# Kernel tuning notes

Measured on AMD Instinct MI355X. Metric: run time of the kernel, lower is better.

The kernel has to match this reference:

```python
import jax, jax.numpy as jnp
import numpy as np

N, T, I_TEXT, H, P = 64, 1024, 512, 512, 256


def setup_inputs() -> dict:
    key = jax.random.key(0)
    ks = jax.random.split(key, 7)
    s = 0.05  # keep recurrent dynamics stable
    return {
        "text_encoding": jax.random.normal(ks[0], (N, T, I_TEXT), jnp.float32),
        "text_lengths": jnp.full((N,), T, dtype=jnp.int32),
        "W_ih": jax.random.normal(ks[1], (3 * H, I_TEXT + P), jnp.float32) * s,
        "W_hh": jax.random.normal(ks[2], (3 * H, H), jnp.float32) * s,
        "b_ih": jax.random.normal(ks[3], (3 * H,), jnp.float32) * s,
        "b_hh": jax.random.normal(ks[4], (3 * H,), jnp.float32) * s,
        "W_p": jax.random.normal(ks[5], (P, H), jnp.float32) * s,
        "b_p": jax.random.normal(ks[6], (P,), jnp.float32) * s,
    }


def reference(text_encoding, text_lengths, W_ih, W_hh, b_ih, b_hh, W_p, b_p):
    n, t, _ = text_encoding.shape
    h_dim = W_hh.shape[1]
    p_dim = W_p.shape[0]
    xs = jnp.transpose(text_encoding, (1, 0, 2))  # [T, N, I_text]

    def step(carry, x):
        h, prev = carry  # h: [N,H] GRU hidden, prev: [N,P] last projected prosody vec
        inp = jnp.concatenate([x, prev], axis=-1)          # [N, I_text+P]
        gi = inp @ W_ih.T + b_ih                           # [N, 3H]
        gh = h @ W_hh.T + b_hh                             # [N, 3H]
        i_r, i_z, i_n = jnp.split(gi, 3, axis=-1)
        h_r, h_z, h_n = jnp.split(gh, 3, axis=-1)
        r = jax.nn.sigmoid(i_r + h_r)
        z = jax.nn.sigmoid(i_z + h_z)
        g = jnp.tanh(i_n + r * h_n)
        h_new = (1.0 - z) * g + z * h
        pred = h_new @ W_p.T + b_p                         # [N, P]
        return (h_new, pred), pred

    h0 = jnp.zeros((n, h_dim), text_encoding.dtype)
    p0 = jnp.zeros((n, p_dim), text_encoding.dtype)
    _, preds = jax.lax.scan(step, (h0, p0), xs)            # [T, N, P]
    return jnp.transpose(preds, (1, 0, 2))                 # [N, T, P]
```

## Files before the change

### kernel.cpp

```cpp
#include <hip/hip_runtime.h>
#include <hip/hip_bf16.h>


typedef short short8 __attribute__((ext_vector_type(8)));
typedef float f32x4 __attribute__((ext_vector_type(4)));

__device__ __forceinline__ unsigned short f2bf(float f) {
  __hip_bfloat16 h = __float2bfloat16(f);
  return *reinterpret_cast<unsigned short*>(&h);
}

__global__ void k_zero(unsigned int* __restrict__ p, int n) {
  int i = blockIdx.x * 256 + threadIdx.x;
  if (i < n) p[i] = 0u;
}

__global__ void k_fold(const float* __restrict__ W_ih, const float* __restrict__ W_hh,
                       const float* __restrict__ W_p, const float* __restrict__ b_p,
                       float* __restrict__ W_big, float* __restrict__ v_bp) {
  int idx = blockIdx.x * 256 + threadIdx.x;
  int i = idx >> 9;
  int j = idx & 511;
  const float* wip = W_ih + (long)i * 768 + 512;
  float q = 0.f;
  for (int k = 0; k < 256; ++k) q = fmaf(wip[k], W_p[k * 512 + j], q);
  if (i < 1024) {
    W_big[(long)i * 512 + j] = W_hh[(long)i * 512 + j] + q;
  } else {
    W_big[(long)i * 512 + j] = q;
    W_big[(long)(i + 512) * 512 + j] = W_hh[(long)i * 512 + j];
  }
  if (j == 0) {
    float s = 0.f;
    for (int k = 0; k < 256; ++k) s = fmaf(b_p[k], wip[k], s);
    v_bp[i] = s;
  }
}

__global__ void k_pack(const float* __restrict__ W_big, const float* __restrict__ W_ih,
                       const float* __restrict__ W_p,
                       unsigned short* __restrict__ Wr, unsigned short* __restrict__ Wx) {
  long e = (long)blockIdx.x * 256 + threadIdx.x;
  if (e < 1572864) {
    int k = (int)(e & 511);
    int cc = (int)((e >> 9) & 15);
    int rest = (int)(e >> 13);
    int T = rest % 3, b = rest / 3;
    int j = b * 8 + (cc & 7);
    bool hi = cc >= 8;
    float v;
    if (T == 0)      v = W_big[(long)(hi ? 512 + j : j) * 512 + k];
    else if (T == 1) v = W_big[(long)(hi ? 1536 + j : 1024 + j) * 512 + k];
    else             v = (cc < 4) ? W_p[(long)(b * 4 + cc) * 512 + k] : 0.f;
    Wr[e] = f2bf(v);
  } else {
    long e2 = e - 1572864;
    int g = (int)(e2 >> 9), k = (int)(e2 & 511);
    Wx[e2] = f2bf(W_ih[(long)g * 768 + k]);
  }
}

__global__ __launch_bounds__(256, 1) void k_persist(
    const float* __restrict__ x,
    const unsigned short* __restrict__ Wr, const unsigned short* __restrict__ Wx,
    const float* __restrict__ b_ih, const float* __restrict__ b_hh,
    const float* __restrict__ v_bp, const float* __restrict__ b_p,
    unsigned short* __restrict__ Hbf,
    float* __restrict__ gix,
    float* __restrict__ out,
    unsigned int* __restrict__ flags,
    unsigned int* __restrict__ gen, unsigned int* __restrict__ dead) {
  const int tid = threadIdx.x;
  const int blk = blockIdx.x;
  const int w = tid >> 6, lane = tid & 63, c = lane & 15, q = lane >> 4;
  __shared__ unsigned short xls[16][536];
  bool alive = true;
  unsigned int round = 0;

  auto barrier = [&](unsigned int rnd) {
    __syncthreads();
    if (tid == 0 && alive)
      __hip_atomic_store(&flags[blk * 16], rnd, __ATOMIC_RELEASE, __HIP_MEMORY_SCOPE_AGENT);
    if (blk == 0) {
      if (tid < 160 && alive) {
        int spins = 0;
        while (__hip_atomic_load(&flags[tid * 16], __ATOMIC_RELAXED,
                                 __HIP_MEMORY_SCOPE_AGENT) < rnd) {
          __builtin_amdgcn_s_sleep(1);
          if ((++spins & 2047) == 0) {
            if (__hip_atomic_load(dead, __ATOMIC_RELAXED, __HIP_MEMORY_SCOPE_AGENT)) {
              alive = false; break;
            }
            if (spins > 1000000) {
              __hip_atomic_store(dead, 1u, __ATOMIC_RELAXED, __HIP_MEMORY_SCOPE_AGENT);
              alive = false; break;
            }
          }
        }
      }
      __syncthreads();
      if (tid == 0 && alive)
        __hip_atomic_store(gen, rnd, __ATOMIC_RELEASE, __HIP_MEMORY_SCOPE_AGENT);
    }
    if (tid == 0 && alive) {
      int spins = 0;
      while (__hip_atomic_load(gen, __ATOMIC_RELAXED, __HIP_MEMORY_SCOPE_AGENT) < rnd) {
        __builtin_amdgcn_s_sleep(1);
        if ((++spins & 2047) == 0) {
          if (__hip_atomic_load(dead, __ATOMIC_RELAXED, __HIP_MEMORY_SCOPE_AGENT)) {
            alive = false; break;
          }
          if (spins > 1000000) {
            __hip_atomic_store(dead, 1u, __ATOMIC_RELAXED, __HIP_MEMORY_SCOPE_AGENT);
            alive = false; break;
          }
        }
      }
      __threadfence();
    }
    __syncthreads();
  };

  if (blk < 64) {
    const int b = blk, j0 = b * 8, n0 = w * 16;
    const int pcol = b * 4 + (c & 3);
    short8 wr0[16], wr1[16], wr2[16];
#pragma unroll
    for (int ki = 0; ki < 16; ++ki) {
      wr0[ki] = *(const short8*)(Wr + (((long)(b * 3 + 0) * 16 + c) * 512 + ki * 32 + q * 8));
      wr1[ki] = *(const short8*)(Wr + (((long)(b * 3 + 1) * 16 + c) * 512 + ki * 32 + q * 8));
      wr2[ki] = *(const short8*)(Wr + (((long)(b * 3 + 2) * 16 + c) * 512 + ki * 32 + q * 8));
    }
    const int jj = j0 + (c & 7);
    const float bihr = b_ih[jj],        bhhr = b_hh[jj],        vbr = v_bp[jj];
    const float bihz = b_ih[512 + jj],  bhhz = b_hh[512 + jj],  vbz = v_bp[512 + jj];
    const float bihn = b_ih[1024 + jj], bhhn = b_hh[1024 + jj], vbn = v_bp[1024 + jj];
    const float bp = b_p[pcol];
    float hprev[4] = {0.f, 0.f, 0.f, 0.f};

    barrier(++round);

    for (int t = 0; t <= 1024; ++t) {
      const int cur = t & 1;
      float gr[4], gz[4], gn[4];
      if (t < 1024) {
        const float* gp = gix + (long)cur * 98304;
#pragma unroll
        for (int r = 0; r < 4; ++r) {
          long nb = (long)(n0 + q * 4 + r) * 1536 + jj;
          gr[r] = gp[nb]; gz[r] = gp[nb + 512]; gn[r] = gp[nb + 1024];
        }
      }
      const unsigned short* hb = Hbf + (long)cur * 32768 + (long)(n0 + c) * 512 + q * 8;
      f32x4 a0{0.f, 0.f, 0.f, 0.f}, a1 = a0, a2 = a0;
#pragma unroll
      for (int ki = 0; ki < 16; ++ki) {
        short8 ah = *(const short8*)(hb + ki * 32);
        a0 = __builtin_amdgcn_mfma_f32_16x16x32_bf16(ah, wr0[ki], a0, 0, 0, 0);
        a1 = __builtin_amdgcn_mfma_f32_16x16x32_bf16(ah, wr1[ki], a1, 0, 0, 0);
        a2 = __builtin_amdgcn_mfma_f32_16x16x32_bf16(ah, wr2[ki], a2, 0, 0, 0);
      }
      if (t >= 1 && c < 4) {
#pragma unroll
        for (int r = 0; r < 4; ++r)
          out[((long)(n0 + q * 4 + r) * 1024 + (t - 1)) * 256 + pcol] = a2[r] + bp;
      }
      if (t == 1024) break;

      const float vb_r = t ? vbr : 0.f, vb_z = t ? vbz : 0.f, vb_n = t ? vbn : 0.f;
#pragma unroll
      for (int r = 0; r < 4; ++r) {
        float pz  = __shfl_xor(a0[r], 8);
        float pnh = __shfl_xor(a1[r], 8);
        if (c < 8) {
          float rr = 1.f / (1.f + __expf(-(a0[r] + gr[r] + bihr + bhhr + vb_r)));
          float zz = 1.f / (1.f + __expf(-(pz + gz[r] + bihz + bhhz + vb_z)));
          float gg = tanhf(a1[r] + gn[r] + bihn + vb_n + rr * (pnh + bhhn));
          float hn = (1.f - zz) * gg + zz * hprev[r];
          hprev[r] = hn;
          Hbf[(long)(cur ^ 1) * 32768 + (long)(n0 + q * 4 + r) * 512 + (j0 + c)] = f2bf(hn);
        }
      }
      barrier(++round);
    }
  } else {
    const int idx = blk - 64, mi = idx & 3, ji = idx >> 2;
    short8 wx[16];
#pragma unroll
    for (int ki = 0; ki < 16; ++ki)
      wx[ki] = *(const short8*)(Wx + (((long)(ji * 4 + w) * 16 + c) * 512 + ki * 32 + q * 8));
    const int col = ji * 64 + w * 16 + c;
    const int srow = tid >> 4, scb = (tid & 15) * 32;

    auto produce = [&](int tt) {
      const float* xs = x + ((long)(16 * mi + srow) * 1024 + tt) * 512 + scb;
#pragma unroll
      for (int cc = 0; cc < 4; ++cc) {
        float4 fa = *(const float4*)(xs + cc * 8);
        float4 fb = *(const float4*)(xs + cc * 8 + 4);
        short8 sv;
        sv[0] = f2bf(fa.x); sv[1] = f2bf(fa.y); sv[2] = f2bf(fa.z); sv[3] = f2bf(fa.w);
        sv[4] = f2bf(fb.x); sv[5] = f2bf(fb.y); sv[6] = f2bf(fb.z); sv[7] = f2bf(fb.w);
        *(short8*)&xls[srow][scb + cc * 8] = sv;
      }
      __syncthreads();
      f32x4 acc{0.f, 0.f, 0.f, 0.f};
#pragma unroll
      for (int ki = 0; ki < 16; ++ki) {
        short8 ax = *(const short8*)&xls[c][ki * 32 + q * 8];
        acc = __builtin_amdgcn_mfma_f32_16x16x32_bf16(ax, wx[ki], acc, 0, 0, 0);
      }
      float* gp = gix + (long)(tt & 1) * 98304;
#pragma unroll
      for (int r = 0; r < 4; ++r)
        gp[(long)(16 * mi + q * 4 + r) * 1536 + col] = acc[r];
    };

    produce(0);
    barrier(++round);
    for (int t = 0; t < 1024; ++t) {
      if (t + 1 < 1024) produce(t + 1);
      barrier(++round);
    }
  }
}

extern "C" void kernel_launch(void* const* d_in, const int* in_sizes, int n_in,
                              void* d_out, int out_size, void* d_ws, size_t ws_size,
                              hipStream_t stream) {
  const float* x    = (const float*)d_in[0];
  const float* W_ih = (const float*)d_in[2];
  const float* W_hh = (const float*)d_in[3];
  const float* b_ih = (const float*)d_in[4];
  const float* b_hh = (const float*)d_in[5];
  const float* W_p  = (const float*)d_in[6];
  const float* b_p  = (const float*)d_in[7];
  float* out = (float*)d_out;

  constexpr size_t OFF_WBIG = 0;
  constexpr size_t OFF_VBP  = 4194304;
  constexpr size_t OFF_WR   = 4202496;
  constexpr size_t OFF_WX   = 7348224;
  constexpr size_t OFF_HBF  = 8921088;
  constexpr size_t OFF_GIX  = 9052160;
  constexpr size_t OFF_FLG  = 9838592;
  constexpr size_t OFF_GEN  = 9854976;
  constexpr size_t WS_NEED  = 9855104;
  if (ws_size < WS_NEED) return;

  char* ws = (char*)d_ws;
  float* W_big        = (float*)(ws + OFF_WBIG);
  float* v_bp         = (float*)(ws + OFF_VBP);
  unsigned short* Wr  = (unsigned short*)(ws + OFF_WR);
  unsigned short* Wx  = (unsigned short*)(ws + OFF_WX);
  unsigned short* Hbf = (unsigned short*)(ws + OFF_HBF);
  float* gix          = (float*)(ws + OFF_GIX);
  unsigned int* flags = (unsigned int*)(ws + OFF_FLG);
  unsigned int* gen   = (unsigned int*)(ws + OFF_GEN);
  unsigned int* dead  = (unsigned int*)(ws + OFF_GEN + 64);

  k_zero<<<913, 256, 0, stream>>>((unsigned int*)(ws + OFF_HBF), 233504);
  k_fold<<<3072, 256, 0, stream>>>(W_ih, W_hh, W_p, b_p, W_big, v_bp);
  k_pack<<<9216, 256, 0, stream>>>(W_big, W_ih, W_p, Wr, Wx);
  k_persist<<<160, 256, 0, stream>>>(x, Wr, Wx, b_ih, b_hh, v_bp, b_p,
                                     Hbf, gix, out, flags, gen, dead);
}
```

Measured before the change: 12.88 ms.

## Fuse input projection into recurrent blocks and use all-to-all flag barrier

Drops the 96 separate producer blocks and the gix global buffer. Each of the 64 recurrent blocks now computes its own slice of the input projection from LDS-resident bf16 weights, and does so between publishing its flag and waiting, so that work overlaps the barrier latency. The two-level barrier (block 0 gathers, then broadcasts a gen counter) becomes a direct poll of all 64 flags. Hidden-state loads and stores use cache-bypassing inline asm, tanh is built from exp and rcp, and the launch shrinks to 64 blocks. The trade-off is extra per-block projection work and reliance on relaxed atomics plus an explicit vmcnt wait for memory ordering.

```diff
diff --git a/kernel.cpp b/kernel.cpp
--- a/kernel.cpp
+++ b/kernel.cpp
@@ -55,56 +55,167 @@
     Wr[e] = f2bf(v);
   } else {
     long e2 = e - 1572864;
-    int g = (int)(e2 >> 9), k = (int)(e2 & 511);
-    Wx[e2] = f2bf(W_ih[(long)g * 768 + k]);
+    int k = (int)(e2 & 511);
+    int cc = (int)((e2 >> 9) & 15);
+    int rest = (int)(e2 >> 13);
+    int T = rest & 1, b = rest >> 1;
+    float v = 0.f;
+    if (T == 0) {
+      int row = (cc < 8) ? (b * 8 + cc) : (512 + b * 8 + (cc - 8));
+      v = W_ih[(long)row * 768 + k];
+    } else if (cc < 8) {
+      v = W_ih[(long)(1024 + b * 8 + cc) * 768 + k];
+    }
+    Wx[e2] = f2bf(v);
   }
 }
 
 __global__ __launch_bounds__(256, 1) void k_persist(
     const float* __restrict__ x,
-    const unsigned short* __restrict__ Wr, const unsigned short* __restrict__ Wx,
+    const unsigned short* __restrict__ Wr, const unsigned short* __restrict__ Wxr,
     const float* __restrict__ b_ih, const float* __restrict__ b_hh,
     const float* __restrict__ v_bp, const float* __restrict__ b_p,
     unsigned short* __restrict__ Hbf,
-    float* __restrict__ gix,
     float* __restrict__ out,
     unsigned int* __restrict__ flags,
-    unsigned int* __restrict__ gen, unsigned int* __restrict__ dead) {
+    unsigned int* __restrict__ dead) {
   const int tid = threadIdx.x;
-  const int blk = blockIdx.x;
+  const int b = blockIdx.x;
   const int w = tid >> 6, lane = tid & 63, c = lane & 15, q = lane >> 4;
-  __shared__ unsigned short xls[16][536];
+  const int j0 = b * 8, n0 = w * 16, jj = j0 + (c & 7), pcol = b * 4 + (c & 3);
+
+  __shared__ unsigned short wxl[32 * 528];
+
+  short8 wr0[16], wr1[16], wr2[16];
+#pragma unroll
+  for (int ki = 0; ki < 16; ++ki) {
+    wr0[ki] = *(const short8*)(Wr + (((long)(b * 3 + 0) * 16 + c) * 512 + ki * 32 + q * 8));
+    wr1[ki] = *(const short8*)(Wr + (((long)(b * 3 + 1) * 16 + c) * 512 + ki * 32 + q * 8));
+    wr2[ki] = *(const short8*)(Wr + (((long)(b * 3 + 2) * 16 + c) * 512 + ki * 32 + q * 8));
+  }
+  {
+    const unsigned short* src = Wxr + (long)b * 16384;
+    int row = tid >> 3, ch = tid & 7;
+#pragma unroll
+    for (int i = 0; i < 8; ++i) {
+      int col = ch * 64 + i * 8;
+      *(short8*)&wxl[row * 528 + col] = *(const short8*)(src + row * 512 + col);
+    }
+  }
+
+  const float bihr = b_ih[jj],        bhhr = b_hh[jj],        vbr = v_bp[jj];
+  const float bihz = b_ih[512 + jj],  bhhz = b_hh[512 + jj],  vbz = v_bp[512 + jj];
+  const float bihn = b_ih[1024 + jj], bhhn = b_hh[1024 + jj], vbn = v_bp[1024 + jj];
+  const float bp = b_p[pcol];
+  float hprev[4] = {0.f, 0.f, 0.f, 0.f};
+  f32x4 gp0{0.f, 0.f, 0.f, 0.f}, gp1 = gp0;
   bool alive = true;
-  unsigned int round = 0;
-
-  auto barrier = [&](unsigned int rnd) {
+
+  __syncthreads();
+
+  auto produce = [&](int tt) {
+    f32x4 p0{0.f, 0.f, 0.f, 0.f}, p1 = p0;
+    const float* xr = x + ((long)(n0 + c) * 1024 + tt) * 512 + q * 8;
+#pragma unroll
+    for (int ki = 0; ki < 16; ++ki) {
+      float4 f0 = *(const float4*)(xr + ki * 32);
+      float4 f1 = *(const float4*)(xr + ki * 32 + 4);
+      short8 ax;
+      ax[0] = f2bf(f0.x); ax[1] = f2bf(f0.y); ax[2] = f2bf(f0.z); ax[3] = f2bf(f0.w);
+      ax[4] = f2bf(f1.x); ax[5] = f2bf(f1.y); ax[6] = f2bf(f1.z); ax[7] = f2bf(f1.w);
+      short8 b0 = *(const short8*)&wxl[c * 528 + ki * 32 + q * 8];
+      short8 b1 = *(const short8*)&wxl[(16 + c) * 528 + ki * 32 + q * 8];
+      p0 = __builtin_amdgcn_mfma_f32_16x16x32_bf16(ax, b0, p0, 0, 0, 0);
+      p1 = __builtin_amdgcn_mfma_f32_16x16x32_bf16(ax, b1, p1, 0, 0, 0);
+    }
+    gp0 = p0; gp1 = p1;
+  };
+
+  produce(0);
+
+  for (int t = 0; t <= 1024; ++t) {
+    const int cur = t & 1;
+    const unsigned short* hb = Hbf + (long)cur * 32768 + (long)(n0 + c) * 512 + q * 8;
+    short8 h0, h1, h2, h3, h4, h5, h6, h7, h8, h9, hA, hB, hC, hD, hE, hF;
+    asm volatile(
+        "global_load_dwordx4 %[o0], %[a], off sc0 sc1\n\t"
+        "global_load_dwordx4 %[o1], %[a], off offset:64 sc0 sc1\n\t"
+        "global_load_dwordx4 %[o2], %[a], off offset:128 sc0 sc1\n\t"
+        "global_load_dwordx4 %[o3], %[a], off offset:192 sc0 sc1\n\t"
+        "global_load_dwordx4 %[o4], %[a], off offset:256 sc0 sc1\n\t"
+        "global_load_dwordx4 %[o5], %[a], off offset:320 sc0 sc1\n\t"
+        "global_load_dwordx4 %[o6], %[a], off offset:384 sc0 sc1\n\t"
+        "global_load_dwordx4 %[o7], %[a], off offset:448 sc0 sc1\n\t"
+        "global_load_dwordx4 %[o8], %[a], off offset:512 sc0 sc1\n\t"
+        "global_load_dwordx4 %[o9], %[a], off offset:576 sc0 sc1\n\t"
+        "global_load_dwordx4 %[oA], %[a], off offset:640 sc0 sc1\n\t"
+        "global_load_dwordx4 %[oB], %[a], off offset:704 sc0 sc1\n\t"
+        "global_load_dwordx4 %[oC], %[a], off offset:768 sc0 sc1\n\t"
+        "global_load_dwordx4 %[oD], %[a], off offset:832 sc0 sc1\n\t"
+        "global_load_dwordx4 %[oE], %[a], off offset:896 sc0 sc1\n\t"
+        "global_load_dwordx4 %[oF], %[a], off offset:960 sc0 sc1\n\t"
+        "s_waitcnt vmcnt(0)"
+        : [o0]"=&v"(h0), [o1]"=&v"(h1), [o2]"=&v"(h2), [o3]"=&v"(h3),
+          [o4]"=&v"(h4), [o5]"=&v"(h5), [o6]"=&v"(h6), [o7]"=&v"(h7),
+          [o8]"=&v"(h8), [o9]"=&v"(h9), [oA]"=&v"(hA), [oB]"=&v"(hB),
+          [oC]"=&v"(hC), [oD]"=&v"(hD), [oE]"=&v"(hE), [oF]"=&v"(hF)
+        : [a]"v"(hb)
+        : "memory");
+
+    f32x4 a0{0.f, 0.f, 0.f, 0.f}, a1 = a0, a2 = a0;
+#define RK(H, K)                                                          \
+    a0 = __builtin_amdgcn_mfma_f32_16x16x32_bf16(H, wr0[K], a0, 0, 0, 0); \
+    a1 = __builtin_amdgcn_mfma_f32_16x16x32_bf16(H, wr1[K], a1, 0, 0, 0); \
+    a2 = __builtin_amdgcn_mfma_f32_16x16x32_bf16(H, wr2[K], a2, 0, 0, 0);
+    RK(h0, 0)  RK(h1, 1)  RK(h2, 2)  RK(h3, 3)
+    RK(h4, 4)  RK(h5, 5)  RK(h6, 6)  RK(h7, 7)
+    RK(h8, 8)  RK(h9, 9)  RK(hA, 10) RK(hB, 11)
+    RK(hC, 12) RK(hD, 13) RK(hE, 14) RK(hF, 15)
+#undef RK
+
+    if (t >= 1 && c < 4) {
+#pragma unroll
+      for (int r = 0; r < 4; ++r)
+        out[((long)(n0 + q * 4 + r) * 1024 + (t - 1)) * 256 + pcol] = a2[r] + bp;
+    }
+    if (t == 1024) break;
+
+    const float cR = t ? (bihr + bhhr + vbr) : (bihr + bhhr);
+    const float cZ = t ? (bihz + bhhz + vbz) : (bihz + bhhz);
+    const float cN = t ? (bihn + vbn) : bihn;
+    float s0x[4], s1x[4];
+#pragma unroll
+    for (int r = 0; r < 4; ++r) { s0x[r] = a0[r] + gp0[r]; s1x[r] = a1[r] + gp1[r]; }
+    unsigned short* hw = Hbf + (long)(cur ^ 1) * 32768 + (long)(n0 + q * 4) * 512 + jj;
+#pragma unroll
+    for (int r = 0; r < 4; ++r) {
+      float ps0 = __shfl_xor(s0x[r], 8);
+      float ps1 = __shfl_xor(s1x[r], 8);
+      if (c < 8) {
+        float rr = __builtin_amdgcn_rcpf(1.f + __expf(-(s0x[r] + cR)));
+        float zz = __builtin_amdgcn_rcpf(1.f + __expf(-(ps0 + cZ)));
+        float aa = s1x[r] + cN + rr * (ps1 + bhhn);
+        float gg = 1.f - 2.f * __builtin_amdgcn_rcpf(1.f + __expf(2.f * aa));
+        float hn = (1.f - zz) * gg + zz * hprev[r];
+        hprev[r] = hn;
+        unsigned short hv = f2bf(hn);
+        unsigned short* pr = hw + r * 512;
+        asm volatile("global_store_short %0, %1, off sc0 sc1" :: "v"(pr), "v"(hv) : "memory");
+      }
+    }
+
+    asm volatile("s_waitcnt vmcnt(0)" ::: "memory");
     __syncthreads();
+    const unsigned int rnd = (unsigned int)t + 1u;
     if (tid == 0 && alive)
-      __hip_atomic_store(&flags[blk * 16], rnd, __ATOMIC_RELEASE, __HIP_MEMORY_SCOPE_AGENT);
-    if (blk == 0) {
-      if (tid < 160 && alive) {
-        int spins = 0;
-        while (__hip_atomic_load(&flags[tid * 16], __ATOMIC_RELAXED,
-                                 __HIP_MEMORY_SCOPE_AGENT) < rnd) {
-          __builtin_amdgcn_s_sleep(1);
-          if ((++spins & 2047) == 0) {
-            if (__hip_atomic_load(dead, __ATOMIC_RELAXED, __HIP_MEMORY_SCOPE_AGENT)) {
-              alive = false; break;
-            }
-            if (spins > 1000000) {
-              __hip_atomic_store(dead, 1u, __ATOMIC_RELAXED, __HIP_MEMORY_SCOPE_AGENT);
-              alive = false; break;
-            }
-          }
-        }
-      }
-      __syncthreads();
-      if (tid == 0 && alive)
-        __hip_atomic_store(gen, rnd, __ATOMIC_RELEASE, __HIP_MEMORY_SCOPE_AGENT);
-    }
-    if (tid == 0 && alive) {
+      __hip_atomic_store(&flags[b * 16], rnd, __ATOMIC_RELAXED, __HIP_MEMORY_SCOPE_AGENT);
+
+    if (t < 1023) produce(t + 1);
+
+    if (tid < 64 && alive) {
       int spins = 0;
-      while (__hip_atomic_load(gen, __ATOMIC_RELAXED, __HIP_MEMORY_SCOPE_AGENT) < rnd) {
+      while (__hip_atomic_load(&flags[tid * 16], __ATOMIC_RELAXED,
+                               __HIP_MEMORY_SCOPE_AGENT) < rnd) {
         __builtin_amdgcn_s_sleep(1);
         if ((++spins & 2047) == 0) {
           if (__hip_atomic_load(dead, __ATOMIC_RELAXED, __HIP_MEMORY_SCOPE_AGENT)) {
@@ -116,112 +227,8 @@
           }
         }
       }
-      __threadfence();
     }
     __syncthreads();
-  };
-
-  if (blk < 64) {
-    const int b = blk, j0 = b * 8, n0 = w * 16;
-    const int pcol = b * 4 + (c & 3);
-    short8 wr0[16], wr1[16], wr2[16];
-#pragma unroll
-    for (int ki = 0; ki < 16; ++ki) {
-      wr0[ki] = *(const short8*)(Wr + (((long)(b * 3 + 0) * 16 + c) * 512 + ki * 32 + q * 8));
-      wr1[ki] = *(const short8*)(Wr + (((long)(b * 3 + 1) * 16 + c) * 512 + ki * 32 + q * 8));
-      wr2[ki] = *(const short8*)(Wr + (((long)(b * 3 + 2) * 16 + c) * 512 + ki * 32 + q * 8));
-    }
-    const int jj = j0 + (c & 7);
-    const float bihr = b_ih[jj],        bhhr = b_hh[jj],        vbr = v_bp[jj];
-    const float bihz = b_ih[512 + jj],  bhhz = b_hh[512 + jj],  vbz = v_bp[512 + jj];
-    const float bihn = b_ih[1024 + jj], bhhn = b_hh[1024 + jj], vbn = v_bp[1024 + jj];
-    const float bp = b_p[pcol];
-    float hprev[4] = {0.f, 0.f, 0.f, 0.f};
-
-    barrier(++round);
-
-    for (int t = 0; t <= 1024; ++t) {
-      const int cur = t & 1;
-      float gr[4], gz[4], gn[4];
-      if (t < 1024) {
-        const float* gp = gix + (long)cur * 98304;
-#pragma unroll
-        for (int r = 0; r < 4; ++r) {
-          long nb = (long)(n0 + q * 4 + r) * 1536 + jj;
-          gr[r] = gp[nb]; gz[r] = gp[nb + 512]; gn[r] = gp[nb + 1024];
-        }
-      }
-      const unsigned short* hb = Hbf + (long)cur * 32768 + (long)(n0 + c) * 512 + q * 8;
-      f32x4 a0{0.f, 0.f, 0.f, 0.f}, a1 = a0, a2 = a0;
-#pragma unroll
-      for (int ki = 0; ki < 16; ++ki) {
-        short8 ah = *(const short8*)(hb + ki * 32);
-        a0 = __builtin_amdgcn_mfma_f32_16x16x32_bf16(ah, wr0[ki], a0, 0, 0, 0);
-        a1 = __builtin_amdgcn_mfma_f32_16x16x32_bf16(ah, wr1[ki], a1, 0, 0, 0);
-        a2 = __builtin_amdgcn_mfma_f32_16x16x32_bf16(ah, wr2[ki], a2, 0, 0, 0);
-      }
-      if (t >= 1 && c < 4) {
-#pragma unroll
-        for (int r = 0; r < 4; ++r)
-          out[((long)(n0 + q * 4 + r) * 1024 + (t - 1)) * 256 + pcol] = a2[r] + bp;
-      }
-      if (t == 1024) break;
-
-      const float vb_r = t ? vbr : 0.f, vb_z = t ? vbz : 0.f, vb_n = t ? vbn : 0.f;
-#pragma unroll
-      for (int r = 0; r < 4; ++r) {
-        float pz  = __shfl_xor(a0[r], 8);
-        float pnh = __shfl_xor(a1[r], 8);
-        if (c < 8) {
-          float rr = 1.f / (1.f + __expf(-(a0[r] + gr[r] + bihr + bhhr + vb_r)));
-          float zz = 1.f / (1.f + __expf(-(pz + gz[r] + bihz + bhhz + vb_z)));
-          float gg = tanhf(a1[r] + gn[r] + bihn + vb_n + rr * (pnh + bhhn));
-          float hn = (1.f - zz) * gg + zz * hprev[r];
-          hprev[r] = hn;
-          Hbf[(long)(cur ^ 1) * 32768 + (long)(n0 + q * 4 + r) * 512 + (j0 + c)] = f2bf(hn);
-        }
-      }
-      barrier(++round);
-    }
-  } else {
-    const int idx = blk - 64, mi = idx & 3, ji = idx >> 2;
-    short8 wx[16];
-#pragma unroll
-    for (int ki = 0; ki < 16; ++ki)
-      wx[ki] = *(const short8*)(Wx + (((long)(ji * 4 + w) * 16 + c) * 512 + ki * 32 + q * 8));
-    const int col = ji * 64 + w * 16 + c;
-    const int srow = tid >> 4, scb = (tid & 15) * 32;
-
-    auto produce = [&](int tt) {
-      const float* xs = x + ((long)(16 * mi + srow) * 1024 + tt) * 512 + scb;
-#pragma unroll
-      for (int cc = 0; cc < 4; ++cc) {
-        float4 fa = *(const float4*)(xs + cc * 8);
-        float4 fb = *(const float4*)(xs + cc * 8 + 4);
-        short8 sv;
-        sv[0] = f2bf(fa.x); sv[1] = f2bf(fa.y); sv[2] = f2bf(fa.z); sv[3] = f2bf(fa.w);
-        sv[4] = f2bf(fb.x); sv[5] = f2bf(fb.y); sv[6] = f2bf(fb.z); sv[7] = f2bf(fb.w);
-        *(short8*)&xls[srow][scb + cc * 8] = sv;
-      }
-      __syncthreads();
-      f32x4 acc{0.f, 0.f, 0.f, 0.f};
-#pragma unroll
-      for (int ki = 0; ki < 16; ++ki) {
-        short8 ax = *(const short8*)&xls[c][ki * 32 + q * 8];
-        acc = __builtin_amdgcn_mfma_f32_16x16x32_bf16(ax, wx[ki], acc, 0, 0, 0);
-      }
-      float* gp = gix + (long)(tt & 1) * 98304;
-#pragma unroll
-      for (int r = 0; r < 4; ++r)
-        gp[(long)(16 * mi + q * 4 + r) * 1536 + col] = acc[r];
-    };
-
-    produce(0);
-    barrier(++round);
-    for (int t = 0; t < 1024; ++t) {
-      if (t + 1 < 1024) produce(t + 1);
-      barrier(++round);
-    }
   }
 }
 
@@ -240,28 +247,25 @@
   constexpr size_t OFF_WBIG = 0;
   constexpr size_t OFF_VBP  = 4194304;
   constexpr size_t OFF_WR   = 4202496;
-  constexpr size_t OFF_WX   = 7348224;
-  constexpr size_t OFF_HBF  = 8921088;
-  constexpr size_t OFF_GIX  = 9052160;
-  constexpr size_t OFF_FLG  = 9838592;
-  constexpr size_t OFF_GEN  = 9854976;
-  constexpr size_t WS_NEED  = 9855104;
+  constexpr size_t OFF_WXR  = 7348224;
+  constexpr size_t OFF_HBF  = 9445376;
+  constexpr size_t OFF_FLG  = 9576448;
+  constexpr size_t OFF_DEAD = 9580544;
+  constexpr size_t WS_NEED  = 9580608;
   if (ws_size < WS_NEED) return;
 
   char* ws = (char*)d_ws;
   float* W_big        = (float*)(ws + OFF_WBIG);
   float* v_bp         = (float*)(ws + OFF_VBP);
   unsigned short* Wr  = (unsigned short*)(ws + OFF_WR);
-  unsigned short* Wx  = (unsigned short*)(ws + OFF_WX);
+  unsigned short* Wxr = (unsigned short*)(ws + OFF_WXR);
   unsigned short* Hbf = (unsigned short*)(ws + OFF_HBF);
-  float* gix          = (float*)(ws + OFF_GIX);
   unsigned int* flags = (unsigned int*)(ws + OFF_FLG);
-  unsigned int* gen   = (unsigned int*)(ws + OFF_GEN);
-  unsigned int* dead  = (unsigned int*)(ws + OFF_GEN + 64);
-
-  k_zero<<<913, 256, 0, stream>>>((unsigned int*)(ws + OFF_HBF), 233504);
+  unsigned int* dead  = (unsigned int*)(ws + OFF_DEAD);
+
+  k_zero<<<133, 256, 0, stream>>>((unsigned int*)(ws + OFF_HBF), 33808);
   k_fold<<<3072, 256, 0, stream>>>(W_ih, W_hh, W_p, b_p, W_big, v_bp);
-  k_pack<<<9216, 256, 0, stream>>>(W_big, W_ih, W_p, Wr, Wx);
-  k_persist<<<160, 256, 0, stream>>>(x, Wr, Wx, b_ih, b_hh, v_bp, b_p,
-                                     Hbf, gix, out, flags, gen, dead);
-}
+  k_pack<<<10240, 256, 0, stream>>>(W_big, W_ih, W_p, Wr, Wxr);
+  k_persist<<<64, 256, 0, stream>>>(x, Wr, Wxr, b_ih, b_hh, v_bp, b_p,
+                                    Hbf, out, flags, dead);
+}
```

Result: no change. 13.03 ms (+1.2%).
